# Kernel optimization log

Measured on AMD Instinct MI355X. Metric: run time of the kernel, lower is better.

## Reference

```python
import jax, jax.numpy as jnp
import numpy as np

B, T, C = 1, 4096, 1024   # batch, seq, n_embd
E, K = 64, 8              # num_experts, router top-k
G, TG = 8, 4              # n_group, topk_group
H, HS = 512, 2048         # expert hidden, shared-expert hidden
STD = 0.02


def setup_inputs() -> dict:
    key = jax.random.key(0)
    ks = jax.random.split(key, 9)
    return {
        "x": jax.random.normal(ks[0], (B, T, C), jnp.float32),
        "router_w": jax.random.normal(ks[1], (E, C), jnp.float32) * (C ** -0.5),
        "e_bias": jnp.zeros((E,), jnp.float32),  # e_score_correction_bias buffer
        "gate_w": jax.random.normal(ks[2], (E, C, H), jnp.float32) * STD,
        "up_w": jax.random.normal(ks[3], (E, C, H), jnp.float32) * STD,
        "down_w": jax.random.normal(ks[4], (E, H, C), jnp.float32) * STD,
        "sh_gate_w": jax.random.normal(ks[5], (C, HS), jnp.float32) * STD,
        "sh_up_w": jax.random.normal(ks[6], (C, HS), jnp.float32) * STD,
        "sh_down_w": jax.random.normal(ks[7], (HS, C), jnp.float32) * STD,
    }


def _route(xf, router_w, e_bias):
    # grouped sigmoid top-k routing with score-correction bias (group_limited_greedy)
    S = xf.shape[0]
    scores = jax.nn.sigmoid(xf @ router_w.T)          # [S,E], raw sigmoid scores
    sb = scores + e_bias                               # biased scores (selection only)
    epg = E // G
    # per-group score = sum of top (K // topk_group) biased scores in that group
    grp = jax.lax.top_k(sb.reshape(S, G, epg), K // TG)[0].sum(-1)   # [S,G]
    gidx = jax.lax.top_k(grp, TG)[1]                                 # [S,TG]
    gmask = jnp.zeros((S, G), bool).at[jnp.arange(S)[:, None], gidx].set(True)
    emask = jnp.repeat(gmask, epg, axis=1)                           # [S,E]
    masked = jnp.where(emask, sb, -jnp.inf)
    topk_idx = jax.lax.top_k(masked, K)[1]                           # [S,K]
    w = jnp.take_along_axis(scores, topk_idx, axis=1)                # raw scores gathered
    w = w / (w.sum(-1, keepdims=True) + 1e-20)                       # norm_topk_prob
    return topk_idx, w


def reference(x, router_w, e_bias, gate_w, up_w, down_w, sh_gate_w, sh_up_w, sh_down_w):
    Bq, Tq, Cq = x.shape
    xf = x.reshape(Bq * Tq, Cq)
    # always-on shared expert (SwiGLU)
    shared = (jax.nn.silu(xf @ sh_gate_w) * (xf @ sh_up_w)) @ sh_down_w
    topk_idx, w = _route(xf, router_w, e_bias)
    fe = topk_idx.reshape(-1)                          # [S*K] expert id per routed row
    order = jnp.argsort(fe, stable=True)               # sort rows by expert (grouped)
    tok = order // K                                   # source token of each sorted row
    sorted_x = xf[tok]                                 # [S*K, C]
    group_sizes = jnp.bincount(fe, length=E).astype(jnp.int32)
    # grouped GEMMs (== torch._grouped_mm / bmm-over-buckets in the original)
    g = jax.lax.ragged_dot(sorted_x, gate_w, group_sizes)
    u = jax.lax.ragged_dot(sorted_x, up_w, group_sizes)
    h = jax.nn.silu(g) * u
    o = jax.lax.ragged_dot(h, down_w, group_sizes)     # [S*K, C]
    o = o * w.reshape(-1)[order][:, None]              # weight by routing prob
    routed = jnp.zeros_like(xf).at[tok].add(o)         # combine back per token
    return (shared + routed).reshape(Bq, Tq, Cq)
```

## Files before the change

### kernel.cpp

```cpp
#include <hip/hip_runtime.h>
#include <hip/hip_bf16.h>
#include <stdint.h>


#define S_TOK 4096
#define C_DIM 1024
#define E_NUM 64
#define H_DIM 512
#define HS_DIM 2048
#define ROWS_TOTAL (S_TOK * 8)
#define T_TILES 320

typedef __attribute__((ext_vector_type(8))) short short8;
typedef __attribute__((ext_vector_type(4))) float f32x4;

static __device__ __forceinline__ unsigned short f2bf(float f) {
    union { float f; uint32_t u; } v; v.f = f;
    uint32_t u = v.u;
    u += 0x7fffu + ((u >> 16) & 1u);
    return (unsigned short)(u >> 16);
}

static __device__ __forceinline__ void gl2lds16(const void* g, void* l) {
    __builtin_amdgcn_global_load_lds(
        (const __attribute__((address_space(1))) uint32_t*)g,
        (__attribute__((address_space(3))) uint32_t*)l, 16, 0, 0);
}

__global__ __launch_bounds__(256)
void router_scores_k(const float* __restrict__ x, const float* __restrict__ rw,
                     float* __restrict__ scores, int* __restrict__ counts) {
    if (blockIdx.x == 0 && threadIdx.x < E_NUM) counts[threadIdx.x] = 0;
    int t0 = blockIdx.x * 32;
    __shared__ float xs[32][36];
    __shared__ float wsm[64][36];
    int t = threadIdx.x;
    int tx = t & 15, ty = t >> 4;
    float acc[2][4] = {};
    for (int k0 = 0; k0 < C_DIM; k0 += 32) {
        {
            int r = t >> 3, c = t & 7;
            *(float4*)&xs[r][c * 4] = *(const float4*)(x + (size_t)(t0 + r) * C_DIM + k0 + c * 4);
        }
        #pragma unroll
        for (int i = 0; i < 2; i++) {
            int idx = t + 256 * i;
            int r = idx >> 3, c = idx & 7;
            *(float4*)&wsm[r][c * 4] = *(const float4*)(rw + (size_t)r * C_DIM + k0 + c * 4);
        }
        __syncthreads();
        #pragma unroll
        for (int kk = 0; kk < 32; kk += 4) {
            float4 a0 = *(const float4*)&xs[ty * 2 + 0][kk];
            float4 a1 = *(const float4*)&xs[ty * 2 + 1][kk];
            #pragma unroll
            for (int j = 0; j < 4; j++) {
                float4 b = *(const float4*)&wsm[tx * 4 + j][kk];
                acc[0][j] += a0.x * b.x + a0.y * b.y + a0.z * b.z + a0.w * b.w;
                acc[1][j] += a1.x * b.x + a1.y * b.y + a1.z * b.z + a1.w * b.w;
            }
        }
        __syncthreads();
    }
    #pragma unroll
    for (int i = 0; i < 2; i++)
        #pragma unroll
        for (int j = 0; j < 4; j++)
            scores[(size_t)(t0 + ty * 2 + i) * E_NUM + tx * 4 + j] =
                1.f / (1.f + __expf(-acc[i][j]));
}

__global__ __launch_bounds__(256)
void topk_k(const float* __restrict__ scores, const float* __restrict__ ebias,
            int* __restrict__ topk_idx, float* __restrict__ topk_w,
            int* __restrict__ counts) {
    int t = blockIdx.x * 4 + (threadIdx.x >> 6);
    int e = threadIdx.x & 63;
    float sc = scores[(size_t)t * E_NUM + e];
    float sb = sc + ebias[e];
    float m1 = sb, m2 = -1e30f;
    #pragma unroll
    for (int off = 1; off <= 4; off <<= 1) {
        float o1 = __shfl_xor(m1, off);
        float o2 = __shfl_xor(m2, off);
        float hi = fmaxf(m1, o1), lo = fminf(m1, o1);
        m2 = fmaxf(lo, fmaxf(m2, o2));
        m1 = hi;
    }
    float grp = m1 + m2;
    float grpv[8];
    #pragma unroll
    for (int g = 0; g < 8; g++) grpv[g] = __shfl(grp, g * 8);
    unsigned gsel = 0;
    #pragma unroll
    for (int k = 0; k < 4; k++) {
        float best = -1e30f; int bi = 0;
        #pragma unroll
        for (int g = 0; g < 8; g++)
            if (!((gsel >> g) & 1) && grpv[g] > best) { best = grpv[g]; bi = g; }
        gsel |= 1u << bi;
    }
    float val = ((gsel >> (e >> 3)) & 1) ? sb : -1e30f;
    int idx[8]; float sv[8]; float wsum = 0.f;
    #pragma unroll
    for (int k = 0; k < 8; k++) {
        uint32_t u = __float_as_uint(val);
        uint32_t mu = (u & 0x80000000u) ? ~u : (u | 0x80000000u);
        unsigned long long key = ((unsigned long long)mu << 6) | (unsigned long long)(63 - e);
        #pragma unroll
        for (int off = 32; off; off >>= 1) {
            unsigned long long ok = __shfl_xor(key, off);
            if (ok > key) key = ok;
        }
        int win = 63 - (int)(key & 63ull);
        idx[k] = win;
        sv[k] = __shfl(sc, win);
        wsum += sv[k];
        if (e == win) val = -1e30f;
    }
    float inv = 1.f / (wsum + 1e-20f);
    if (e < 8) {
        topk_idx[t * 8 + e] = idx[e];
        topk_w[t * 8 + e] = sv[e] * inv;
        atomicAdd(&counts[idx[e]], 1);
    }
}

__global__ void scan_k(const int* __restrict__ counts, int* __restrict__ base,
                       int* __restrict__ cursor, int* __restrict__ tile_e,
                       int* __restrict__ tile_m0) {
    int e = threadIdx.x;
    int c = counts[e];
    int s = c;
    #pragma unroll
    for (int off = 1; off < 64; off <<= 1) {
        int o = __shfl_up(s, off);
        if (e >= off) s += o;
    }
    int ex = s - c;
    base[e] = ex;
    cursor[e] = ex;
    int nt = (c + 127) >> 7;
    int ts = nt;
    #pragma unroll
    for (int off = 1; off < 64; off <<= 1) {
        int o = __shfl_up(ts, off);
        if (e >= off) ts += o;
    }
    int tb = ts - nt;
    for (int i = 0; i < nt; i++) { tile_e[tb + i] = e; tile_m0[tb + i] = i * 128; }
    int total = __shfl(ts, 63);
    for (int j = total + e; j < T_TILES; j += 64) tile_e[j] = -1;
}

__global__ void scatter_k(const int* __restrict__ topk_idx, const float* __restrict__ topk_w,
                          int* __restrict__ cursor, int* __restrict__ row_token,
                          float* __restrict__ row_wgt, int* __restrict__ pos_of) {
    int i = blockIdx.x * blockDim.x + threadIdx.x;
    int e = topk_idx[i];
    int pos = atomicAdd(&cursor[e], 1);
    row_token[pos] = i >> 3;
    row_wgt[pos] = topk_w[i];
    pos_of[i] = pos;
}

__global__ __launch_bounds__(256)
void combine_k(const float* __restrict__ O, const int* __restrict__ pos_of,
               float* __restrict__ out) {
    int t = blockIdx.x;
    int c = threadIdx.x;
    float4 s = ((const float4*)(out + (size_t)t * C_DIM))[c];
    int p[8];
    #pragma unroll
    for (int k = 0; k < 8; k++) p[k] = pos_of[t * 8 + k];
    #pragma unroll
    for (int k = 0; k < 8; k++) {
        float4 v = ((const float4*)(O + (size_t)p[k] * C_DIM))[c];
        s.x += v.x; s.y += v.y; s.z += v.z; s.w += v.w;
    }
    ((float4*)(out + (size_t)t * C_DIM))[c] = s;
}

__global__ void cvt_bf16_k(const float* __restrict__ in, unsigned short* __restrict__ out, int n8) {
    int i = blockIdx.x * blockDim.x + threadIdx.x;
    if (i >= n8) return;
    float4 v0 = ((const float4*)in)[2 * i];
    float4 v1 = ((const float4*)in)[2 * i + 1];
    unsigned short t[8] = { f2bf(v0.x), f2bf(v0.y), f2bf(v0.z), f2bf(v0.w),
                            f2bf(v1.x), f2bf(v1.y), f2bf(v1.z), f2bf(v1.w) };
    ((uint4*)out)[i] = *(uint4*)t;
}

template<bool FUSED, bool GATHER, bool WL, int EPI>
__global__ __launch_bounds__(256, 3)
void gemm2_k(const short* __restrict__ A, const float* __restrict__ B1f,
             const float* __restrict__ B2f, void* __restrict__ Cout,
             int M, int N, int K,
             const int* __restrict__ counts, const int* __restrict__ base,
             const int* __restrict__ row_token, const float* __restrict__ row_wgt,
             const int* __restrict__ tile_e, const int* __restrict__ tile_m0) {
    constexpr int BN = FUSED ? 64 : 128;
    constexpr int NJ = FUSED ? 2 : 4;
    constexpr int BS = BN * 32;

    int e = 0, m0, Mrows, rowbase = 0;
    if (WL) {
        e = tile_e[blockIdx.y];
        if (e < 0) return;
        m0 = tile_m0[blockIdx.y];
        Mrows = counts[e];
        rowbase = base[e];
    } else {
        m0 = blockIdx.y * 128;
        Mrows = M;
    }
    int n0 = blockIdx.x * BN;
    const float* B1 = B1f + (WL ? (size_t)e * N * K : 0);
    const float* B2 = FUSED ? (B2f + (WL ? (size_t)e * N * K : 0)) : nullptr;

    __shared__ short As[3 * 4096];
    __shared__ short Bs1[2 * BS];
    __shared__ short Bs2[FUSED ? 2 * BS : 16];

    int tid = threadIdx.x;
    int lane = tid & 63, w = tid >> 6;
    int wr = w >> 1, wc = w & 1;
    int quad = lane >> 4, l16 = lane & 15;
    int sr = lane >> 2, sc = lane & 3;

    const short* aptr[2];
    #pragma unroll
    for (int i = 0; i < 2; i++) {
        int row = w * 32 + i * 16 + sr;
        int mrow = m0 + row;
        int cl = mrow < Mrows ? mrow : (Mrows - 1);
        size_t arow;
        if (GATHER)  arow = (size_t)row_token[rowbase + cl];
        else if (WL) arow = (size_t)(rowbase + cl);
        else         arow = (size_t)mrow;
        aptr[i] = A + arow * K + sc * 8;
    }

    int nb = tid & 63, kg = tid >> 6;
    const float* b1g = B1 + (size_t)(kg * 8) * N + n0 + nb;
    const float* b2g = FUSED ? (B2 + (size_t)(kg * 8) * N + n0 + nb) : nullptr;
    const int bwr = nb * 32 + ((kg * 8) ^ ((nb & 3) << 3));

    f32x4 acc1[4][NJ] = {};
    f32x4 acc2[FUSED ? 4 : 1][NJ] = {};

    const int nk = K >> 5;

    auto stageA = [&](int slot) {
        #pragma unroll
        for (int i = 0; i < 2; i++) {
            gl2lds16(aptr[i], &As[slot * 4096 + (w * 32 + i * 16) * 32]);
            aptr[i] += 32;
        }
    };
    auto loadB = [&](float (&fb)[2][8]) {
        #pragma unroll
        for (int jj = 0; jj < 8; jj++) fb[0][jj] = b1g[(size_t)jj * N];
        if constexpr (FUSED) {
            #pragma unroll
            for (int jj = 0; jj < 8; jj++) fb[1][jj] = b2g[(size_t)jj * N];
            b2g += (size_t)32 * N;
        } else {
            #pragma unroll
            for (int jj = 0; jj < 8; jj++) fb[1][jj] = b1g[(size_t)jj * N + 64];
        }
        b1g += (size_t)32 * N;
    };
    auto cvtpk = [](float a, float b) -> uint32_t {
        uint32_t r;
        asm("v_cvt_pk_bf16_f32 %0, %1, %2" : "=v"(r) : "v"(a), "v"(b));
        return r;
    };
    auto writeB = [&](int buf, float (&fb)[2][8]) {
        uint32_t w0[4], w1[4];
        #pragma unroll
        for (int q = 0; q < 4; q++) {
            w0[q] = cvtpk(fb[0][2 * q], fb[0][2 * q + 1]);
            w1[q] = cvtpk(fb[1][2 * q], fb[1][2 * q + 1]);
        }
        *(uint4*)&Bs1[buf * BS + bwr] = *(uint4*)w0;
        if constexpr (FUSED) *(uint4*)&Bs2[buf * BS + bwr] = *(uint4*)w1;
        else                 *(uint4*)&Bs1[buf * BS + bwr + 64 * 32] = *(uint4*)w1;
    };

    float fbA[2][8], fbB[2][8];
    stageA(0);
    if (nk > 1) stageA(1);
    __builtin_amdgcn_sched_barrier(0);
    {
        float fb0[2][8];
        loadB(fb0);
        writeB(0, fb0);
    }
    __builtin_amdgcn_sched_barrier(0);
    if (nk > 1) loadB(fbA);
    asm volatile("s_waitcnt vmcnt(16) lgkmcnt(0)" ::: "memory");
    __builtin_amdgcn_s_barrier();
    __builtin_amdgcn_sched_barrier(0);

    auto kstep = [&](int t, float (&fbIn)[2][8], float (&fbOut)[2][8]) {
        int slot = t % 3;
        int bbuf = t & 1;
        bool pf = (t + 2 < nk);
        if (pf) { stageA((t + 2) % 3); loadB(fbOut); }

        short8 a[4], b1[NJ], b2[NJ];
        #pragma unroll
        for (int i = 0; i < 4; i++)
            a[i] = *(const short8*)&As[slot * 4096 + (wr * 64 + i * 16 + l16) * 32 + quad * 8];
        #pragma unroll
        for (int j = 0; j < NJ; j++) {
            int row = wc * (BN / 2) + j * 16 + l16;
            int ro = row * 32 + ((quad * 8) ^ ((row & 3) << 3));
            b1[j] = *(const short8*)&Bs1[bbuf * BS + ro];
            if constexpr (FUSED) b2[j] = *(const short8*)&Bs2[bbuf * BS + ro];
        }
        #pragma unroll
        for (int i = 0; i < 4; i++)
            #pragma unroll
            for (int j = 0; j < NJ; j++) {
                acc1[i][j] = __builtin_amdgcn_mfma_f32_16x16x32_bf16(a[i], b1[j], acc1[i][j], 0, 0, 0);
                if (FUSED)
                    acc2[i][j] = __builtin_amdgcn_mfma_f32_16x16x32_bf16(a[i], b2[j], acc2[i][j], 0, 0, 0);
            }
        if (t + 1 < nk) {
            writeB((t + 1) & 1, fbIn);
            if (pf) asm volatile("s_waitcnt vmcnt(18) lgkmcnt(0)" ::: "memory");
            else    asm volatile("s_waitcnt vmcnt(0) lgkmcnt(0)" ::: "memory");
            __builtin_amdgcn_s_barrier();
            __builtin_amdgcn_sched_barrier(0);
        }
    };

    for (int t = 0; t < nk; t += 2) {
        kstep(t, fbA, fbB);
        if (t + 1 < nk) kstep(t + 1, fbB, fbA);
    }

    constexpr int CB = BN / 2;
    #pragma unroll
    for (int i = 0; i < 4; i++) {
        #pragma unroll
        for (int rr = 0; rr < 4; rr++) {
            int row = m0 + wr * 64 + i * 16 + quad * 4 + rr;
            if (row >= Mrows) continue;
            size_t orow = WL ? (size_t)(rowbase + row) : (size_t)row;
            float scl = 0.f;
            if (EPI == 2) scl = row_wgt[rowbase + row];
            #pragma unroll
            for (int j = 0; j < NJ; j++) {
                int n = n0 + wc * CB + j * 16 + l16;
                float v = acc1[i][j][rr];
                if (EPI == 0) {
                    float u = acc2[i][j][rr];
                    float h = v / (1.f + __expf(-v)) * u;
                    ((unsigned short*)Cout)[orow * N + n] = f2bf(h);
                } else if (EPI == 1) {
                    ((float*)Cout)[orow * N + n] = v;
                } else {
                    ((float*)Cout)[orow * N + n] = v * scl;
                }
            }
        }
    }
}

extern "C" void kernel_launch(void* const* d_in, const int* in_sizes, int n_in,
                              void* d_out, int out_size, void* d_ws, size_t ws_size,
                              hipStream_t stream) {
    const float* x        = (const float*)d_in[0];
    const float* router_w = (const float*)d_in[1];
    const float* e_bias   = (const float*)d_in[2];
    const float* gate_w   = (const float*)d_in[3];
    const float* up_w     = (const float*)d_in[4];
    const float* down_w   = (const float*)d_in[5];
    const float* sh_gate  = (const float*)d_in[6];
    const float* sh_up    = (const float*)d_in[7];
    const float* sh_down  = (const float*)d_in[8];
    float* out = (float*)d_out;
    char* ws = (char*)d_ws;

    int*   counts    = (int*)(ws);
    int*   base      = (int*)(ws + 256);
    int*   cursor    = (int*)(ws + 512);
    int*   topk_idx  = (int*)(ws + 1024);
    float* topk_w    = (float*)(ws + 1024 + 131072);
    int*   row_token = (int*)(ws + 1024 + 2 * 131072);
    float* row_wgt   = (float*)(ws + 1024 + 3 * 131072);
    float* scoresbuf = (float*)(ws + 1024 + 4 * 131072);
    int*   pos_of    = (int*)(ws + 1664 * 1024);
    int*   tile_e    = (int*)(ws + 1800 * 1024);
    int*   tile_m0   = (int*)(ws + 1808 * 1024);
    const size_t MB = 1u << 20;
    unsigned short* xb = (unsigned short*)(ws + 2 * MB);
    unsigned short* Hs = (unsigned short*)(ws + 10 * MB);
    unsigned short* Hr = (unsigned short*)(ws + 26 * MB);
    float*          O  = (float*)(ws + 70 * MB);

    router_scores_k<<<S_TOK / 32, 256, 0, stream>>>(x, router_w, scoresbuf, counts);
    topk_k<<<S_TOK / 4, 256, 0, stream>>>(scoresbuf, e_bias, topk_idx, topk_w, counts);
    scan_k<<<1, 64, 0, stream>>>(counts, base, cursor, tile_e, tile_m0);
    scatter_k<<<ROWS_TOTAL / 256, 256, 0, stream>>>(topk_idx, topk_w, cursor, row_token, row_wgt, pos_of);

    cvt_bf16_k<<<S_TOK * C_DIM / 8 / 256, 256, 0, stream>>>(x, xb, S_TOK * C_DIM / 8);

    gemm2_k<true, false, false, 0><<<dim3(HS_DIM / 64, S_TOK / 128, 1), 256, 0, stream>>>(
        (const short*)xb, sh_gate, sh_up, Hs,
        S_TOK, HS_DIM, C_DIM, nullptr, nullptr, nullptr, nullptr, nullptr, nullptr);
    gemm2_k<false, false, false, 1><<<dim3(C_DIM / 128, S_TOK / 128, 1), 256, 0, stream>>>(
        (const short*)Hs, sh_down, nullptr, out,
        S_TOK, C_DIM, HS_DIM, nullptr, nullptr, nullptr, nullptr, nullptr, nullptr);

    gemm2_k<true, true, true, 0><<<dim3(H_DIM / 64, T_TILES, 1), 256, 0, stream>>>(
        (const short*)xb, gate_w, up_w, Hr,
        0, H_DIM, C_DIM, counts, base, row_token, row_wgt, tile_e, tile_m0);
    gemm2_k<false, false, true, 2><<<dim3(C_DIM / 128, T_TILES, 1), 256, 0, stream>>>(
        (const short*)Hr, down_w, nullptr, O,
        0, C_DIM, H_DIM, counts, base, row_token, row_wgt, tile_e, tile_m0);

    combine_k<<<S_TOK, 256, 0, stream>>>(O, pos_of, out);
}
```

Measured before the change: 868.5 us.

## Load expert weights with vector loads and read LDS via transpose reads

Each thread now loads the fp32 B weights as contiguous float4 chunks along N, instead of 16 strided scalar loads down K. It packs them to bf16 and stores them in a K-major blocked LDS layout. MFMA B operands are then fetched with ds_read_b64_tr_b16 transpose reads rather than swizzled row reads. The aim is fewer global load instructions and cheaper B staging. In exchange it adds an explicit lgkmcnt wait before the MFMAs and drops the manual vmcnt waits, relying on the compiler to order the A and B global loads correctly.

Result: slower. 887.1 us (+2.1%).

```diff
diff --git a/kernel.cpp b/kernel.cpp
--- a/kernel.cpp
+++ b/kernel.cpp
@@ -13,6 +13,7 @@
 
 typedef __attribute__((ext_vector_type(8))) short short8;
 typedef __attribute__((ext_vector_type(4))) float f32x4;
+typedef __attribute__((ext_vector_type(2))) unsigned int uint2v;
 
 static __device__ __forceinline__ unsigned short f2bf(float f) {
     union { float f; uint32_t u; } v; v.f = f;
@@ -25,6 +26,18 @@
     __builtin_amdgcn_global_load_lds(
         (const __attribute__((address_space(1))) uint32_t*)g,
         (__attribute__((address_space(3))) uint32_t*)l, 16, 0, 0);
+}
+
+static __device__ __forceinline__ uint32_t cvtpk(float a, float b) {
+    uint32_t r;
+    asm("v_cvt_pk_bf16_f32 %0, %1, %2" : "=v"(r) : "v"(a), "v"(b));
+    return r;
+}
+
+static __device__ __forceinline__ uint2v tr64(unsigned addr) {
+    uint2v r;
+    asm volatile("ds_read_b64_tr_b16 %0, %1" : "=v"(r) : "v"(addr));
+    return r;
 }
 
 __global__ __launch_bounds__(256)
@@ -201,6 +214,7 @@
              const int* __restrict__ tile_e, const int* __restrict__ tile_m0) {
     constexpr int BN = FUSED ? 64 : 128;
     constexpr int NJ = FUSED ? 2 : 4;
+    constexpr int CH = BN / 16;
     constexpr int BS = BN * 32;
 
     int e = 0, m0, Mrows, rowbase = 0;
@@ -241,10 +255,11 @@
         aptr[i] = A + arow * K + sc * 8;
     }
 
-    int nb = tid & 63, kg = tid >> 6;
-    const float* b1g = B1 + (size_t)(kg * 8) * N + n0 + nb;
-    const float* b2g = FUSED ? (B2 + (size_t)(kg * 8) * N + n0 + nb) : nullptr;
-    const int bwr = nb * 32 + ((kg * 8) ^ ((nb & 3) << 3));
+    int bk = tid >> 3;
+    int bn = FUSED ? (tid & 7) * 8 : (tid & 7) * 16;
+    const float* b1g = B1 + (size_t)bk * N + n0 + bn;
+    const float* b2g = FUSED ? (B2 + (size_t)bk * N + n0 + bn) : nullptr;
+    const int wbase = ((bk >> 2) * CH + (bn >> 4)) * 64 + (bk & 3) * 16 + (bn & 15);
 
     f32x4 acc1[4][NJ] = {};
     f32x4 acc2[FUSED ? 4 : 1][NJ] = {};
@@ -258,56 +273,65 @@
             aptr[i] += 32;
         }
     };
-    auto loadB = [&](float (&fb)[2][8]) {
-        #pragma unroll
-        for (int jj = 0; jj < 8; jj++) fb[0][jj] = b1g[(size_t)jj * N];
+    auto loadB = [&](float (&fb)[16]) {
         if constexpr (FUSED) {
-            #pragma unroll
-            for (int jj = 0; jj < 8; jj++) fb[1][jj] = b2g[(size_t)jj * N];
+            *(float4*)&fb[0]  = *(const float4*)(b1g);
+            *(float4*)&fb[4]  = *(const float4*)(b1g + 4);
+            *(float4*)&fb[8]  = *(const float4*)(b2g);
+            *(float4*)&fb[12] = *(const float4*)(b2g + 4);
             b2g += (size_t)32 * N;
         } else {
-            #pragma unroll
-            for (int jj = 0; jj < 8; jj++) fb[1][jj] = b1g[(size_t)jj * N + 64];
+            *(float4*)&fb[0]  = *(const float4*)(b1g);
+            *(float4*)&fb[4]  = *(const float4*)(b1g + 4);
+            *(float4*)&fb[8]  = *(const float4*)(b1g + 8);
+            *(float4*)&fb[12] = *(const float4*)(b1g + 12);
         }
         b1g += (size_t)32 * N;
     };
-    auto cvtpk = [](float a, float b) -> uint32_t {
-        uint32_t r;
-        asm("v_cvt_pk_bf16_f32 %0, %1, %2" : "=v"(r) : "v"(a), "v"(b));
-        return r;
+    auto writeB = [&](int buf, float (&fb)[16]) {
+        uint32_t pk[8];
+        #pragma unroll
+        for (int q = 0; q < 8; q++) pk[q] = cvtpk(fb[2 * q], fb[2 * q + 1]);
+        if constexpr (FUSED) {
+            *(uint2v*)&Bs1[buf * BS + wbase]     = *(uint2v*)&pk[0];
+            *(uint2v*)&Bs1[buf * BS + wbase + 4] = *(uint2v*)&pk[2];
+            *(uint2v*)&Bs2[buf * BS + wbase]     = *(uint2v*)&pk[4];
+            *(uint2v*)&Bs2[buf * BS + wbase + 4] = *(uint2v*)&pk[6];
+        } else {
+            *(uint2v*)&Bs1[buf * BS + wbase]      = *(uint2v*)&pk[0];
+            *(uint2v*)&Bs1[buf * BS + wbase + 4]  = *(uint2v*)&pk[2];
+            *(uint2v*)&Bs1[buf * BS + wbase + 8]  = *(uint2v*)&pk[4];
+            *(uint2v*)&Bs1[buf * BS + wbase + 12] = *(uint2v*)&pk[6];
+        }
     };
-    auto writeB = [&](int buf, float (&fb)[2][8]) {
-        uint32_t w0[4], w1[4];
-        #pragma unroll
-        for (int q = 0; q < 4; q++) {
-            w0[q] = cvtpk(fb[0][2 * q], fb[0][2 * q + 1]);
-            w1[q] = cvtpk(fb[1][2 * q], fb[1][2 * q + 1]);
-        }
-        *(uint4*)&Bs1[buf * BS + bwr] = *(uint4*)w0;
-        if constexpr (FUSED) *(uint4*)&Bs2[buf * BS + bwr] = *(uint4*)w1;
-        else                 *(uint4*)&Bs1[buf * BS + bwr + 64 * 32] = *(uint4*)w1;
+    unsigned trb1 = (unsigned)(size_t)&Bs1[0] + (unsigned)(quad * 2 * CH * 128 + l16 * 8);
+    unsigned trb2 = FUSED ? ((unsigned)(size_t)&Bs2[0] + (unsigned)(quad * 2 * CH * 128 + l16 * 8)) : 0u;
+    auto rdB = [&](unsigned trb, int buf, int nb) -> short8 {
+        unsigned a0 = trb + (unsigned)(buf * BS * 2 + nb * 128);
+        uint2v lo = tr64(a0);
+        uint2v hi = tr64(a0 + CH * 128);
+        union { uint32_t u[4]; short8 s; } u;
+        u.u[0] = lo[0]; u.u[1] = lo[1]; u.u[2] = hi[0]; u.u[3] = hi[1];
+        return u.s;
     };
 
-    float fbA[2][8], fbB[2][8];
+    float fbA[16], fbB[16];
     stageA(0);
     if (nk > 1) stageA(1);
-    __builtin_amdgcn_sched_barrier(0);
     {
-        float fb0[2][8];
+        float fb0[16];
         loadB(fb0);
         writeB(0, fb0);
     }
-    __builtin_amdgcn_sched_barrier(0);
     if (nk > 1) loadB(fbA);
-    asm volatile("s_waitcnt vmcnt(16) lgkmcnt(0)" ::: "memory");
+    asm volatile("s_waitcnt lgkmcnt(0)" ::: "memory");
     __builtin_amdgcn_s_barrier();
     __builtin_amdgcn_sched_barrier(0);
 
-    auto kstep = [&](int t, float (&fbIn)[2][8], float (&fbOut)[2][8]) {
+    auto kstep = [&](int t, float (&fbIn)[16], float (&fbOut)[16]) {
         int slot = t % 3;
         int bbuf = t & 1;
-        bool pf = (t + 2 < nk);
-        if (pf) { stageA((t + 2) % 3); loadB(fbOut); }
+        if (t + 2 < nk) { stageA((t + 2) % 3); loadB(fbOut); }
 
         short8 a[4], b1[NJ], b2[NJ];
         #pragma unroll
@@ -315,11 +339,12 @@
             a[i] = *(const short8*)&As[slot * 4096 + (wr * 64 + i * 16 + l16) * 32 + quad * 8];
         #pragma unroll
         for (int j = 0; j < NJ; j++) {
-            int row = wc * (BN / 2) + j * 16 + l16;
-            int ro = row * 32 + ((quad * 8) ^ ((row & 3) << 3));
-            b1[j] = *(const short8*)&Bs1[bbuf * BS + ro];
-            if constexpr (FUSED) b2[j] = *(const short8*)&Bs2[bbuf * BS + ro];
-        }
+            int nb = wc * (BN / 32) + j;
+            b1[j] = rdB(trb1, bbuf, nb);
+            if constexpr (FUSED) b2[j] = rdB(trb2, bbuf, nb);
+        }
+        asm volatile("s_waitcnt lgkmcnt(0)" ::: "memory");
+        __builtin_amdgcn_sched_barrier(0);
         #pragma unroll
         for (int i = 0; i < 4; i++)
             #pragma unroll
@@ -330,8 +355,7 @@
             }
         if (t + 1 < nk) {
             writeB((t + 1) & 1, fbIn);
-            if (pf) asm volatile("s_waitcnt vmcnt(18) lgkmcnt(0)" ::: "memory");
-            else    asm volatile("s_waitcnt vmcnt(0) lgkmcnt(0)" ::: "memory");
+            asm volatile("s_waitcnt lgkmcnt(0)" ::: "memory");
             __builtin_amdgcn_s_barrier();
             __builtin_amdgcn_sched_barrier(0);
         }
```
